# Kernel optimization log

Measured on AMD Instinct MI355X. Metric: run time of the kernel, lower is better.

The kernel has to match this reference:

```python
import jax, jax.numpy as jnp
import numpy as np

B, T, H, I, O = 64, 1024, 512, 64, 8
NOISE_STD = 0.05
ALPHA = 0.2


def setup_inputs() -> dict:
    key = jax.random.key(0)
    ks = jax.random.split(key, 5)
    return {
        "input": jax.random.normal(ks[0], (B, T, I), dtype=jnp.float32),
        "noise": jax.random.normal(ks[1], (B, T, H), dtype=jnp.float32),
        "wi": jax.random.normal(ks[2], (I, H), dtype=jnp.float32) / np.float32(np.sqrt(H)),
        "si": jnp.ones((I,), jnp.float32),
        # scale so the all-positive effective recurrence |wrec| stays stable over T steps
        "wrec": jax.random.normal(ks[3], (H, H), dtype=jnp.float32) * np.float32(0.5 / H),
        "b": jnp.zeros((H,), jnp.float32),
        "wo": jax.random.normal(ks[4], (H, O), dtype=jnp.float32) / np.float32(H),
        "so": jnp.ones((O,), jnp.float32),
        "wi_mask": jnp.ones((I, H), jnp.float32),
        "wrec_mask": jnp.ones((H, H), jnp.float32),
        "wo_mask": jnp.ones((H, O), jnp.float32),
        "h0": jnp.zeros((H,), jnp.float32),
    }


def reference(input, noise, wi, si, wrec, b, wo, so, wi_mask, wrec_mask, wo_mask, h0):
    batch = input.shape[0]
    # effective weights (constant across timesteps; torch recomputes identical values each step)
    wrec_eff = jnp.abs(wrec) * wrec_mask            # [H, H]
    wi_eff = (wi * si[:, None]) * wi_mask           # [I, H]
    wo_eff = (wo * so[None, :]) * wo_mask           # [H, O]

    h_init = jnp.broadcast_to(h0, (batch, h0.shape[0]))  # [B, H]

    def step(h, xs):
        x_t, n_t = xs                                # [B, I], [B, H]
        r = jax.nn.relu(h)                           # rate from previous state
        h_new = h + NOISE_STD * n_t + ALPHA * (-h + r @ wrec_eff + b + x_t @ wi_eff)
        out_t = jax.nn.relu(h_new) @ wo_eff          # [B, O]
        return h_new, (out_t, h_new)

    xs = (jnp.swapaxes(input, 0, 1), jnp.swapaxes(noise, 0, 1))  # time-major
    _, (outs, hs) = jax.lax.scan(step, h_init, xs)
    output = jnp.swapaxes(outs, 0, 1)                            # [B, T, O]
    trajectories = jnp.concatenate(
        [h_init[:, None, :], jnp.swapaxes(hs, 0, 1)], axis=1     # [B, T+1, H]
    )
    return output, trajectories
```

## Files before the change

kernel.cpp:

```cpp
#include <hip/hip_runtime.h>
#include <hip/hip_bf16.h>
#include <cstddef>
#include <cstdint>

#define BB 64
#define TT 1024
#define HH 512
#define II 64
#define OO 8
#define NOISE_STD 0.05f
#define ALPHA 0.2f

#define G_SLICES 16
#define BT 4
#define NC (BB/BT)
#define K4EXT 160
#define R2STRIDE 328

typedef _Float16 half2_t __attribute__((ext_vector_type(2)));
typedef unsigned int uint32;
typedef uint32 uint4_t __attribute__((ext_vector_type(4)));

#if __has_builtin(__builtin_amdgcn_fdot2)
__device__ __forceinline__ float fdot2f(half2_t a, half2_t b, float c) {
    return __builtin_amdgcn_fdot2(a, b, c, false);
}
#else
__device__ __forceinline__ float fdot2f(half2_t a, half2_t b, float c) {
    return c + (float)a[0] * (float)b[0] + (float)a[1] * (float)b[1];
}
#endif

__device__ __forceinline__ half2_t pkrtz(float a, float b) {
    return __builtin_bit_cast(half2_t, __builtin_amdgcn_cvt_pkrtz(a, b));
}

__device__ __forceinline__ uint4_t load4_sc1(const uint32* p) {
    uint4_t v;
    asm volatile("global_load_dwordx4 %0, %1, off sc1\n\t"
                 "s_waitcnt vmcnt(0)"
                 : "=v"(v) : "v"(p) : "memory");
    return v;
}
__device__ __forceinline__ uint4_t load4_sc0(const uint32* p) {
    uint4_t v;
    asm volatile("global_load_dwordx4 %0, %1, off sc0\n\t"
                 "s_waitcnt vmcnt(0)"
                 : "=v"(v) : "v"(p) : "memory");
    return v;
}
__device__ __forceinline__ void store1_plain(uint32* p, uint32 v) {
    asm volatile("global_store_dword %0, %1, off" :: "v"(p), "v"(v) : "memory");
}

__global__ __launch_bounds__(512, 2)
void rnn_clique(const float* __restrict__ input, const float* __restrict__ noise,
                const float* __restrict__ wi, const float* __restrict__ si,
                const float* __restrict__ wrec, const float* __restrict__ bvec,
                const float* __restrict__ wo, const float* __restrict__ so,
                const float* __restrict__ wi_mask, const float* __restrict__ wrec_mask,
                const float* __restrict__ wo_mask, const float* __restrict__ h0,
                uint32* __restrict__ ex, float* __restrict__ out,
                float* __restrict__ traj)
{
    const int tid  = threadIdx.x;
    const int cq   = blockIdx.x & 15;
    const int sl   = blockIdx.x >> 4;
    const int wv   = tid >> 6;
    const int lane = tid & 63;

    __shared__ half2_t w2[K4EXT * 64];
    __shared__ half2_t r2[BT][R2STRIDE];
    __shared__ float   part[BT][8][32];
    __shared__ half2_t wo2[256];
    __shared__ int     mode_sh;

    uint32* aux = ex + (size_t)NC * 2 * BT * HH;

    if (tid == 0) {
        uint32 xcc;
        asm volatile("s_getreg_b32 %0, hwreg(HW_REG_XCC_ID)" : "=s"(xcc));
        xcc &= 0xFFu;
        __hip_atomic_store(aux + cq * 16 + sl, (1u << 16) | xcc,
                           __ATOMIC_RELAXED, __HIP_MEMORY_SCOPE_AGENT);
    }

    {
        const int c = tid & 31, kg = tid >> 5;
        const int gc = sl * 32 + c;
        for (int m = 0; m < 10; ++m) {
            int k4 = m * 16 + kg;
            float v[4];
            #pragma unroll
            for (int q = 0; q < 4; ++q) {
                int kap = k4 * 4 + q;
                float x;
                if (kap < HH) {
                    x = fabsf(wrec[(size_t)kap * HH + gc]) * wrec_mask[(size_t)kap * HH + gc];
                } else if (kap < HH + II) {
                    int i = kap - HH;
                    x = wi[(size_t)i * HH + gc] * si[i] * wi_mask[(size_t)i * HH + gc];
                } else if (kap == HH + II) {
                    x = bvec[gc];
                } else {
                    x = 0.f;
                }
                v[q] = x;
            }
            w2[k4 * 64 + c * 2]     = pkrtz(v[0], v[1]);
            w2[k4 * 64 + c * 2 + 1] = pkrtz(v[2], v[3]);
        }
    }
    if (sl < OO && tid < 256) {
        int k2 = tid, o = sl;
        float v0 = wo[(size_t)(2 * k2) * OO + o] * so[o] * wo_mask[(size_t)(2 * k2) * OO + o];
        float v1 = wo[(size_t)(2 * k2 + 1) * OO + o] * so[o] * wo_mask[(size_t)(2 * k2 + 1) * OO + o];
        wo2[k2] = pkrtz(v0, v1);
    }
    if (tid < 128) {
        int k4 = tid;
        float v0 = fmaxf(h0[4 * k4 + 0], 0.f), v1 = fmaxf(h0[4 * k4 + 1], 0.f);
        float v2 = fmaxf(h0[4 * k4 + 2], 0.f), v3 = fmaxf(h0[4 * k4 + 3], 0.f);
        half2_t p0 = pkrtz(v0, v1), p1 = pkrtz(v2, v3);
        for (int b = 0; b < BT; ++b) { r2[b][2 * k4] = p0; r2[b][2 * k4 + 1] = p1; }
    }
    if (tid < BT) {
        r2[tid][288] = half2_t{(_Float16)1.f, (_Float16)0.f};
        for (int s = 289; s < R2STRIDE; ++s) r2[tid][s] = half2_t{(_Float16)0.f, (_Float16)0.f};
    }
    if (wv >= 4 && lane < 32) {
        int b = wv - 4, i2 = lane;
        const float* xp = input + ((size_t)(cq * BT + b) * TT + 0) * II + 2 * i2;
        r2[b][256 + i2] = pkrtz(xp[0], xp[1]);
    }

    float h_st = 0.f, n_reg = 0.f;
    float* trajp = nullptr;
    const float* noisep = nullptr;
    uint32* exw = nullptr;
    if (wv < BT && lane < 32) {
        int b = wv, c = lane, gc = sl * 32 + c, bg = cq * BT + b;
        h_st   = h0[gc];
        noisep = noise + (size_t)bg * TT * HH;
        trajp  = traj + (size_t)bg * (TT + 1) * HH;
        n_reg  = noisep[gc];
        trajp[gc] = h_st;
        exw = ex + (size_t)((cq * 2 + 0) * BT + b) * HH + gc;
    }

    if (wv == 0) {
        uint32 v = (1u << 16);
        for (;;) {
            if (lane < 16)
                v = __hip_atomic_load(aux + cq * 16 + lane,
                                      __ATOMIC_RELAXED, __HIP_MEMORY_SCOPE_AGENT);
            if (__ballot((v >> 16) == 1u) == ~0ull) break;
            __builtin_amdgcn_s_sleep(1);
        }
        uint32 myx = v & 0xFFFFu;
        uint32 x0  = __shfl(myx, 0);
        bool eq = (lane < 16) ? (myx == x0) : true;
        if (lane == 0) mode_sh = (__ballot(eq) == ~0ull) ? 1 : 0;
    }
    __syncthreads();
    const bool local_mode = (mode_sh != 0);

    const int c_    = lane & 31;
    const int shalf = lane >> 5;
    const int seg   = wv * 2 + shalf;

    const int gb  = tid >> 7;
    const int k4g = tid & 127;
    uint32* exg0 = ex + (size_t)((cq * 2 + 0) * BT + gb) * HH + (size_t)(4 * k4g);
    const size_t expar = (size_t)BT * HH;

    for (int t = 0; t < TT; ++t) {
        float acc0 = 0.f, acc1 = 0.f, acc2 = 0.f, acc3 = 0.f;
        #pragma unroll
        for (int ch = 0; ch < 5; ++ch) {
            int k2b = seg * 20 + ch * 4;
            int k4b = seg * 10 + ch * 2;
            half2_t w00 = w2[k4b * 64 + c_ * 2];
            half2_t w01 = w2[k4b * 64 + c_ * 2 + 1];
            half2_t w10 = w2[(k4b + 1) * 64 + c_ * 2];
            half2_t w11 = w2[(k4b + 1) * 64 + c_ * 2 + 1];
            {
                half2_t ra = r2[0][k2b], rb = r2[0][k2b + 1], rc = r2[0][k2b + 2], rd = r2[0][k2b + 3];
                acc0 = fdot2f(ra, w00, acc0); acc0 = fdot2f(rb, w01, acc0);
                acc0 = fdot2f(rc, w10, acc0); acc0 = fdot2f(rd, w11, acc0);
            }
            {
                half2_t ra = r2[1][k2b], rb = r2[1][k2b + 1], rc = r2[1][k2b + 2], rd = r2[1][k2b + 3];
                acc1 = fdot2f(ra, w00, acc1); acc1 = fdot2f(rb, w01, acc1);
                acc1 = fdot2f(rc, w10, acc1); acc1 = fdot2f(rd, w11, acc1);
            }
            {
                half2_t ra = r2[2][k2b], rb = r2[2][k2b + 1], rc = r2[2][k2b + 2], rd = r2[2][k2b + 3];
                acc2 = fdot2f(ra, w00, acc2); acc2 = fdot2f(rb, w01, acc2);
                acc2 = fdot2f(rc, w10, acc2); acc2 = fdot2f(rd, w11, acc2);
            }
            {
                half2_t ra = r2[3][k2b], rb = r2[3][k2b + 1], rc = r2[3][k2b + 2], rd = r2[3][k2b + 3];
                acc3 = fdot2f(ra, w00, acc3); acc3 = fdot2f(rb, w01, acc3);
                acc3 = fdot2f(rc, w10, acc3); acc3 = fdot2f(rd, w11, acc3);
            }
        }
        acc0 += __shfl_xor(acc0, 32);
        acc1 += __shfl_xor(acc1, 32);
        acc2 += __shfl_xor(acc2, 32);
        acc3 += __shfl_xor(acc3, 32);
        if (shalf == 0) {
            part[0][wv][c_] = acc0;
            part[1][wv][c_] = acc1;
            part[2][wv][c_] = acc2;
            part[3][wv][c_] = acc3;
        }
        __syncthreads();

        const uint32 tag = (uint32)(t + 1);
        const size_t poff = (size_t)((t + 1) & 1) * expar;

        if (wv < BT && lane < 32) {
            int b = wv, c = lane, gc = sl * 32 + c;
            float mv = 0.f;
            #pragma unroll
            for (int m = 0; m < 8; ++m) mv += part[b][m][c];
            float hn = (1.f - ALPHA) * h_st + ALPHA * mv + NOISE_STD * n_reg;
            h_st = hn;
            uint32 r16 = __builtin_bit_cast(uint32,
                           __builtin_amdgcn_cvt_pkrtz(fmaxf(hn, 0.f), 0.f)) & 0xFFFFu;
            uint32 word = (tag << 16) | r16;
            if (local_mode) {
                store1_plain(exw + poff, word);
            } else {
                __hip_atomic_store(exw + poff, word,
                                   __ATOMIC_RELAXED, __HIP_MEMORY_SCOPE_AGENT);
            }
            trajp[(size_t)(t + 1) * HH + gc] = hn;
            int tn = (t + 1 < TT) ? (t + 1) : (TT - 1);
            n_reg = noisep[(size_t)tn * HH + gc];
        } else if (wv >= 4) {
            if (sl < OO && t > 0) {
                int b = wv - 4;
                int k2 = lane * 4;
                float p = 0.f;
                p = fdot2f(r2[b][k2],     wo2[k2],     p);
                p = fdot2f(r2[b][k2 + 1], wo2[k2 + 1], p);
                p = fdot2f(r2[b][k2 + 2], wo2[k2 + 2], p);
                p = fdot2f(r2[b][k2 + 3], wo2[k2 + 3], p);
                #pragma unroll
                for (int d = 32; d >= 1; d >>= 1) p += __shfl_xor(p, d);
                if (lane == 0) out[((size_t)(cq * BT + b) * TT + (t - 1)) * OO + sl] = p;
            }
            if (lane < 32) {
                int b = wv - 4, i2 = lane;
                int tn = (t + 1 < TT) ? (t + 1) : (TT - 1);
                const float* xp = input + ((size_t)(cq * BT + b) * TT + tn) * II + 2 * i2;
                r2[b][256 + i2] = pkrtz(xp[0], xp[1]);
            }
        }
        __syncthreads();

        {
            const uint32* g0 = exg0 + poff;
            uint4_t w;
            if (local_mode) {
                for (;;) {
                    w = load4_sc0(g0);
                    if ((w[0] >> 16) == tag && (w[1] >> 16) == tag &&
                        (w[2] >> 16) == tag && (w[3] >> 16) == tag) break;
                    __builtin_amdgcn_s_sleep(1);
                }
            } else {
                for (;;) {
                    w = load4_sc1(g0);
                    if ((w[0] >> 16) == tag && (w[1] >> 16) == tag &&
                        (w[2] >> 16) == tag && (w[3] >> 16) == tag) break;
                    __builtin_amdgcn_s_sleep(1);
                }
            }
            uint32 p0 = (w[0] & 0xFFFFu) | (w[1] << 16);
            uint32 p1 = (w[2] & 0xFFFFu) | (w[3] << 16);
            r2[gb][2 * k4g]     = __builtin_bit_cast(half2_t, p0);
            r2[gb][2 * k4g + 1] = __builtin_bit_cast(half2_t, p1);
        }
        __syncthreads();
    }

    if (wv >= 4 && sl < OO) {
        int b = wv - 4;
        int k2 = lane * 4;
        float p = 0.f;
        p = fdot2f(r2[b][k2],     wo2[k2],     p);
        p = fdot2f(r2[b][k2 + 1], wo2[k2 + 1], p);
        p = fdot2f(r2[b][k2 + 2], wo2[k2 + 2], p);
        p = fdot2f(r2[b][k2 + 3], wo2[k2 + 3], p);
        #pragma unroll
        for (int d = 32; d >= 1; d >>= 1) p += __shfl_xor(p, d);
        if (lane == 0) out[((size_t)(cq * BT + b) * TT + (TT - 1)) * OO + sl] = p;
    }
}

extern "C" void kernel_launch(void* const* d_in, const int* in_sizes, int n_in,
                              void* d_out, int out_size, void* d_ws, size_t ws_size,
                              hipStream_t stream) {
    const float* input     = (const float*)d_in[0];
    const float* noise     = (const float*)d_in[1];
    const float* wi        = (const float*)d_in[2];
    const float* si        = (const float*)d_in[3];
    const float* wrec      = (const float*)d_in[4];
    const float* bvec      = (const float*)d_in[5];
    const float* wo        = (const float*)d_in[6];
    const float* so        = (const float*)d_in[7];
    const float* wi_mask   = (const float*)d_in[8];
    const float* wrec_mask = (const float*)d_in[9];
    const float* wo_mask   = (const float*)d_in[10];
    const float* h0        = (const float*)d_in[11];

    float* out  = (float*)d_out;
    float* traj = out + (size_t)BB * TT * OO;
    uint32* ex  = (uint32*)d_ws;

    (void)hipMemsetAsync(d_ws, 0,
        (size_t)(NC * 2 * BT * HH + NC * G_SLICES) * sizeof(uint32), stream);

    rnn_clique<<<dim3(NC * G_SLICES), dim3(512), 0, stream>>>(
        input, noise, wi, si, wrec, bvec, wo, so,
        wi_mask, wrec_mask, wo_mask, h0, ex, out, traj);
}
```

Measured before the change: 1.689 ms.

## Double-buffer recurrent state in LDS, dropping a barrier per step and caching weights

The shared activation buffer r2 becomes two parity buffers. Each step reads one buffer and writes the next step's state and input into the other, so one __syncthreads per timestep is removed. Each lane's recurrent weight slice is loaded into registers once before the time loop instead of being read from LDS every step. Noise is prefetched two steps ahead, and the local-mode spin loop polls a few times before sleeping. This trades extra LDS and VGPR use, and a changed exchange tag and parity scheme, for less per-step synchronization and memory latency on the serial critical path.

After: 1.608 ms. 4.8% less time.

```diff
diff --git a/kernel.cpp b/kernel.cpp
--- a/kernel.cpp
+++ b/kernel.cpp
@@ -70,7 +70,7 @@
     const int lane = tid & 63;
 
     __shared__ half2_t w2[K4EXT * 64];
-    __shared__ half2_t r2[BT][R2STRIDE];
+    __shared__ half2_t r2[2][BT][R2STRIDE];
     __shared__ float   part[BT][8][32];
     __shared__ half2_t wo2[256];
     __shared__ int     mode_sh;
@@ -122,19 +122,20 @@
         float v0 = fmaxf(h0[4 * k4 + 0], 0.f), v1 = fmaxf(h0[4 * k4 + 1], 0.f);
         float v2 = fmaxf(h0[4 * k4 + 2], 0.f), v3 = fmaxf(h0[4 * k4 + 3], 0.f);
         half2_t p0 = pkrtz(v0, v1), p1 = pkrtz(v2, v3);
-        for (int b = 0; b < BT; ++b) { r2[b][2 * k4] = p0; r2[b][2 * k4 + 1] = p1; }
-    }
-    if (tid < BT) {
-        r2[tid][288] = half2_t{(_Float16)1.f, (_Float16)0.f};
-        for (int s = 289; s < R2STRIDE; ++s) r2[tid][s] = half2_t{(_Float16)0.f, (_Float16)0.f};
+        for (int b = 0; b < BT; ++b) { r2[0][b][2 * k4] = p0; r2[0][b][2 * k4 + 1] = p1; }
+    }
+    if (tid < 8) {
+        int par = tid & 1, b = tid >> 1;
+        r2[par][b][288] = half2_t{(_Float16)1.f, (_Float16)0.f};
+        for (int s = 289; s < R2STRIDE; ++s) r2[par][b][s] = half2_t{(_Float16)0.f, (_Float16)0.f};
     }
     if (wv >= 4 && lane < 32) {
         int b = wv - 4, i2 = lane;
         const float* xp = input + ((size_t)(cq * BT + b) * TT + 0) * II + 2 * i2;
-        r2[b][256 + i2] = pkrtz(xp[0], xp[1]);
-    }
-
-    float h_st = 0.f, n_reg = 0.f;
+        r2[0][b][256 + i2] = pkrtz(xp[0], xp[1]);
+    }
+
+    float h_st = 0.f, n_reg = 0.f, n_reg2 = 0.f;
     float* trajp = nullptr;
     const float* noisep = nullptr;
     uint32* exw = nullptr;
@@ -144,8 +145,24 @@
         noisep = noise + (size_t)bg * TT * HH;
         trajp  = traj + (size_t)bg * (TT + 1) * HH;
         n_reg  = noisep[gc];
+        n_reg2 = noisep[(size_t)HH + gc];
         trajp[gc] = h_st;
         exw = ex + (size_t)((cq * 2 + 0) * BT + b) * HH + gc;
+    }
+    __syncthreads();
+
+    const int c_    = lane & 31;
+    const int shalf = lane >> 5;
+    const int seg   = wv * 2 + shalf;
+
+    half2_t wr[5][4];
+    #pragma unroll
+    for (int ch = 0; ch < 5; ++ch) {
+        int k4b = seg * 10 + ch * 2;
+        wr[ch][0] = w2[k4b * 64 + c_ * 2];
+        wr[ch][1] = w2[k4b * 64 + c_ * 2 + 1];
+        wr[ch][2] = w2[(k4b + 1) * 64 + c_ * 2];
+        wr[ch][3] = w2[(k4b + 1) * 64 + c_ * 2 + 1];
     }
 
     if (wv == 0) {
@@ -165,44 +182,37 @@
     __syncthreads();
     const bool local_mode = (mode_sh != 0);
 
-    const int c_    = lane & 31;
-    const int shalf = lane >> 5;
-    const int seg   = wv * 2 + shalf;
-
     const int gb  = tid >> 7;
     const int k4g = tid & 127;
     uint32* exg0 = ex + (size_t)((cq * 2 + 0) * BT + gb) * HH + (size_t)(4 * k4g);
     const size_t expar = (size_t)BT * HH;
 
     for (int t = 0; t < TT; ++t) {
+        const int p = t & 1;
+
         float acc0 = 0.f, acc1 = 0.f, acc2 = 0.f, acc3 = 0.f;
         #pragma unroll
         for (int ch = 0; ch < 5; ++ch) {
             int k2b = seg * 20 + ch * 4;
-            int k4b = seg * 10 + ch * 2;
-            half2_t w00 = w2[k4b * 64 + c_ * 2];
-            half2_t w01 = w2[k4b * 64 + c_ * 2 + 1];
-            half2_t w10 = w2[(k4b + 1) * 64 + c_ * 2];
-            half2_t w11 = w2[(k4b + 1) * 64 + c_ * 2 + 1];
             {
-                half2_t ra = r2[0][k2b], rb = r2[0][k2b + 1], rc = r2[0][k2b + 2], rd = r2[0][k2b + 3];
-                acc0 = fdot2f(ra, w00, acc0); acc0 = fdot2f(rb, w01, acc0);
-                acc0 = fdot2f(rc, w10, acc0); acc0 = fdot2f(rd, w11, acc0);
+                half2_t ra = r2[p][0][k2b], rb = r2[p][0][k2b + 1], rc = r2[p][0][k2b + 2], rd = r2[p][0][k2b + 3];
+                acc0 = fdot2f(ra, wr[ch][0], acc0); acc0 = fdot2f(rb, wr[ch][1], acc0);
+                acc0 = fdot2f(rc, wr[ch][2], acc0); acc0 = fdot2f(rd, wr[ch][3], acc0);
             }
             {
-                half2_t ra = r2[1][k2b], rb = r2[1][k2b + 1], rc = r2[1][k2b + 2], rd = r2[1][k2b + 3];
-                acc1 = fdot2f(ra, w00, acc1); acc1 = fdot2f(rb, w01, acc1);
-                acc1 = fdot2f(rc, w10, acc1); acc1 = fdot2f(rd, w11, acc1);
+                half2_t ra = r2[p][1][k2b], rb = r2[p][1][k2b + 1], rc = r2[p][1][k2b + 2], rd = r2[p][1][k2b + 3];
+                acc1 = fdot2f(ra, wr[ch][0], acc1); acc1 = fdot2f(rb, wr[ch][1], acc1);
+                acc1 = fdot2f(rc, wr[ch][2], acc1); acc1 = fdot2f(rd, wr[ch][3], acc1);
             }
             {
-                half2_t ra = r2[2][k2b], rb = r2[2][k2b + 1], rc = r2[2][k2b + 2], rd = r2[2][k2b + 3];
-                acc2 = fdot2f(ra, w00, acc2); acc2 = fdot2f(rb, w01, acc2);
-                acc2 = fdot2f(rc, w10, acc2); acc2 = fdot2f(rd, w11, acc2);
+                half2_t ra = r2[p][2][k2b], rb = r2[p][2][k2b + 1], rc = r2[p][2][k2b + 2], rd = r2[p][2][k2b + 3];
+                acc2 = fdot2f(ra, wr[ch][0], acc2); acc2 = fdot2f(rb, wr[ch][1], acc2);
+                acc2 = fdot2f(rc, wr[ch][2], acc2); acc2 = fdot2f(rd, wr[ch][3], acc2);
             }
             {
-                half2_t ra = r2[3][k2b], rb = r2[3][k2b + 1], rc = r2[3][k2b + 2], rd = r2[3][k2b + 3];
-                acc3 = fdot2f(ra, w00, acc3); acc3 = fdot2f(rb, w01, acc3);
-                acc3 = fdot2f(rc, w10, acc3); acc3 = fdot2f(rd, w11, acc3);
+                half2_t ra = r2[p][3][k2b], rb = r2[p][3][k2b + 1], rc = r2[p][3][k2b + 2], rd = r2[p][3][k2b + 3];
+                acc3 = fdot2f(ra, wr[ch][0], acc3); acc3 = fdot2f(rb, wr[ch][1], acc3);
+                acc3 = fdot2f(rc, wr[ch][2], acc3); acc3 = fdot2f(rd, wr[ch][3], acc3);
             }
         }
         acc0 += __shfl_xor(acc0, 32);
@@ -217,8 +227,8 @@
         }
         __syncthreads();
 
-        const uint32 tag = (uint32)(t + 1);
-        const size_t poff = (size_t)((t + 1) & 1) * expar;
+        const uint32 tag = (uint32)(t + 2);
+        const size_t poff = (size_t)p * expar;
 
         if (wv < BT && lane < 32) {
             int b = wv, c = lane, gc = sl * 32 + c;
@@ -237,39 +247,40 @@
                                    __ATOMIC_RELAXED, __HIP_MEMORY_SCOPE_AGENT);
             }
             trajp[(size_t)(t + 1) * HH + gc] = hn;
-            int tn = (t + 1 < TT) ? (t + 1) : (TT - 1);
-            n_reg = noisep[(size_t)tn * HH + gc];
+            n_reg = n_reg2;
+            int tn = (t + 2 < TT) ? (t + 2) : (TT - 1);
+            n_reg2 = noisep[(size_t)tn * HH + gc];
         } else if (wv >= 4) {
             if (sl < OO && t > 0) {
                 int b = wv - 4;
                 int k2 = lane * 4;
-                float p = 0.f;
-                p = fdot2f(r2[b][k2],     wo2[k2],     p);
-                p = fdot2f(r2[b][k2 + 1], wo2[k2 + 1], p);
-                p = fdot2f(r2[b][k2 + 2], wo2[k2 + 2], p);
-                p = fdot2f(r2[b][k2 + 3], wo2[k2 + 3], p);
+                float q = 0.f;
+                q = fdot2f(r2[p][b][k2],     wo2[k2],     q);
+                q = fdot2f(r2[p][b][k2 + 1], wo2[k2 + 1], q);
+                q = fdot2f(r2[p][b][k2 + 2], wo2[k2 + 2], q);
+                q = fdot2f(r2[p][b][k2 + 3], wo2[k2 + 3], q);
                 #pragma unroll
-                for (int d = 32; d >= 1; d >>= 1) p += __shfl_xor(p, d);
-                if (lane == 0) out[((size_t)(cq * BT + b) * TT + (t - 1)) * OO + sl] = p;
+                for (int d = 32; d >= 1; d >>= 1) q += __shfl_xor(q, d);
+                if (lane == 0) out[((size_t)(cq * BT + b) * TT + (t - 1)) * OO + sl] = q;
             }
             if (lane < 32) {
                 int b = wv - 4, i2 = lane;
                 int tn = (t + 1 < TT) ? (t + 1) : (TT - 1);
                 const float* xp = input + ((size_t)(cq * BT + b) * TT + tn) * II + 2 * i2;
-                r2[b][256 + i2] = pkrtz(xp[0], xp[1]);
-            }
-        }
-        __syncthreads();
+                r2[p ^ 1][b][256 + i2] = pkrtz(xp[0], xp[1]);
+            }
+        }
 
         {
             const uint32* g0 = exg0 + poff;
             uint4_t w;
+            int spins = 0;
             if (local_mode) {
                 for (;;) {
                     w = load4_sc0(g0);
                     if ((w[0] >> 16) == tag && (w[1] >> 16) == tag &&
                         (w[2] >> 16) == tag && (w[3] >> 16) == tag) break;
-                    __builtin_amdgcn_s_sleep(1);
+                    if (++spins > 8) __builtin_amdgcn_s_sleep(1);
                 }
             } else {
                 for (;;) {
@@ -279,10 +290,10 @@
                     __builtin_amdgcn_s_sleep(1);
                 }
             }
-            uint32 p0 = (w[0] & 0xFFFFu) | (w[1] << 16);
-            uint32 p1 = (w[2] & 0xFFFFu) | (w[3] << 16);
-            r2[gb][2 * k4g]     = __builtin_bit_cast(half2_t, p0);
-            r2[gb][2 * k4g + 1] = __builtin_bit_cast(half2_t, p1);
+            uint32 q0 = (w[0] & 0xFFFFu) | (w[1] << 16);
+            uint32 q1 = (w[2] & 0xFFFFu) | (w[3] << 16);
+            r2[p ^ 1][gb][2 * k4g]     = __builtin_bit_cast(half2_t, q0);
+            r2[p ^ 1][gb][2 * k4g + 1] = __builtin_bit_cast(half2_t, q1);
         }
         __syncthreads();
     }
@@ -290,14 +301,14 @@
     if (wv >= 4 && sl < OO) {
         int b = wv - 4;
         int k2 = lane * 4;
-        float p = 0.f;
-        p = fdot2f(r2[b][k2],     wo2[k2],     p);
-        p = fdot2f(r2[b][k2 + 1], wo2[k2 + 1], p);
-        p = fdot2f(r2[b][k2 + 2], wo2[k2 + 2], p);
-        p = fdot2f(r2[b][k2 + 3], wo2[k2 + 3], p);
+        float q = 0.f;
+        q = fdot2f(r2[0][b][k2],     wo2[k2],     q);
+        q = fdot2f(r2[0][b][k2 + 1], wo2[k2 + 1], q);
+        q = fdot2f(r2[0][b][k2 + 2], wo2[k2 + 2], q);
+        q = fdot2f(r2[0][b][k2 + 3], wo2[k2 + 3], q);
         #pragma unroll
-        for (int d = 32; d >= 1; d >>= 1) p += __shfl_xor(p, d);
-        if (lane == 0) out[((size_t)(cq * BT + b) * TT + (TT - 1)) * OO + sl] = p;
+        for (int d = 32; d >= 1; d >>= 1) q += __shfl_xor(q, d);
+        if (lane == 0) out[((size_t)(cq * BT + b) * TT + (TT - 1)) * OO + sl] = q;
     }
 }
 
```
